# Kernel optimization log

Measured on AMD Instinct MI355X. Metric: run time of the kernel, lower is better.

## Reference

```python
import jax, jax.numpy as jnp
import numpy as np
import math

S = 64.0
M = 0.5
COS_M = math.cos(M)
SIN_M = math.sin(M)
TH = math.cos(math.pi - M)
MM = math.sin(math.pi - M) * M
BATCH = 512
EMBED = 512
NUM_CLASSES = 100000

def setup_inputs() -> dict:
    key = jax.random.key(0)
    k1, k2, k3 = jax.random.split(key, 3)
    inp = jax.random.normal(k1, (BATCH, EMBED), dtype=jnp.float32)
    label = jax.random.randint(k2, (BATCH,), 0, NUM_CLASSES, dtype=jnp.int64)
    # xavier_uniform_ on [num_classes, embedding_size]
    limit = math.sqrt(6.0 / (NUM_CLASSES + EMBED))
    weight = jax.random.uniform(k3, (NUM_CLASSES, EMBED), dtype=jnp.float32,
                                minval=-limit, maxval=limit)
    return {"input": inp, "label": label, "weight": weight}


def reference(input, label, weight):
    # F.normalize(weight) along dim=1 (eps=1e-12), then F.linear
    w_norm = weight / jnp.maximum(jnp.linalg.norm(weight, axis=1, keepdims=True), 1e-12)
    cosine = input @ w_norm.T  # [B, C]
    sine = jnp.sqrt(jnp.clip(1.0 - cosine * cosine, 0.0, 1.0))
    phi = cosine * COS_M - sine * SIN_M
    phi = jnp.where(cosine > TH, phi, cosine - MM)
    one_hot = jax.nn.one_hot(label, NUM_CLASSES, dtype=cosine.dtype)  # [B, C]
    output = (one_hot * phi + (1.0 - one_hot) * cosine) * S
    logp = jax.nn.log_softmax(output, axis=-1)
    # NLLLoss with mean reduction
    loss = -jnp.mean(jnp.take_along_axis(logp, label[:, None], axis=1)[:, 0])
    return (output, loss)
```

## Files before the change

### kernel.cpp

```cpp
#include <hip/hip_runtime.h>

#define NCLS   100000
#define CPAD   100096
#define EMB    512
#define BATCH  512
#define NBN    782
#define NJ     1564

#define S_F     64.0f
#define COS_M_F 0.8775825619f
#define SIN_M_F 0.4794255386f
#define TH_F   (-0.8775825619f)
#define MM_F    0.2397127693f

#define WS_ABF   0ull
#define WS_PMAX  524288ull
#define WS_PSUM  3727360ull
#define WS_NLL   6930432ull
#define WS_EXACT 6932480ull
#define WS_INV   6934528ull
#define WS_WBF   7334912ull

typedef unsigned short ushort_t;
typedef __attribute__((ext_vector_type(8))) short bf16x8;
typedef __attribute__((ext_vector_type(4))) float floatx4;

__device__ __forceinline__ unsigned short f2bf(float f) {
    union { float f; unsigned int u; } c; c.f = f;
    unsigned int r = c.u + 0x7FFFu + ((c.u >> 16) & 1u);
    return (unsigned short)(r >> 16);
}

__device__ __forceinline__ void load_lds16(const void* g, void* l) {
    __builtin_amdgcn_global_load_lds(
        (const __attribute__((address_space(1))) void*)g,
        (__attribute__((address_space(3))) void*)l, 16, 0, 0);
}

__device__ __forceinline__ int xcd_swizzle(int b0, int nwg) {
    const int q = nwg >> 3, r = nwg & 7;
    const int x = b0 & 7, o = b0 >> 3;
    const int base = (x < r) ? x * (q + 1) : r * (q + 1) + (x - r) * q;
    return base + o;
}

__global__ __launch_bounds__(256) void cvt_input_kernel(
    const float* __restrict__ in, ushort_t* __restrict__ Abf) {
    int gid = blockIdx.x * 256 + threadIdx.x;
    float4 f = ((const float4*)in)[gid];
    uint2 u;
    u.x = (unsigned)f2bf(f.x) | ((unsigned)f2bf(f.y) << 16);
    u.y = (unsigned)f2bf(f.z) | ((unsigned)f2bf(f.w) << 16);
    ((uint2*)Abf)[gid] = u;
}

__global__ __launch_bounds__(256) void exact_label_kernel(
    const float* __restrict__ input, const float* __restrict__ W,
    const int* __restrict__ label, float* __restrict__ exact_val) {
    const int t = threadIdx.x;
    const int lane = t & 63;
    const int row = blockIdx.x * 4 + (t >> 6);
    const int lab = label[row];
    const float4* ip = (const float4*)(input + (size_t)row * EMB);
    const float4* wp = (const float4*)(W + (size_t)lab * EMB);
    float4 a0 = ip[lane], a1 = ip[64 + lane];
    float4 b0 = wp[lane], b1 = wp[64 + lane];
    float dot = a0.x*b0.x + a0.y*b0.y + a0.z*b0.z + a0.w*b0.w
              + a1.x*b1.x + a1.y*b1.y + a1.z*b1.z + a1.w*b1.w;
    float ssq = b0.x*b0.x + b0.y*b0.y + b0.z*b0.z + b0.w*b0.w
              + b1.x*b1.x + b1.y*b1.y + b1.z*b1.z + b1.w*b1.w;
    #pragma unroll
    for (int msk = 1; msk < 64; msk <<= 1) {
        dot += __shfl_xor(dot, msk);
        ssq += __shfl_xor(ssq, msk);
    }
    if (lane == 0) {
        float c = dot / fmaxf(sqrtf(ssq), 1e-12f);
        float sine = sqrtf(fmaxf(1.0f - c * c, 0.0f));
        float phi = c * COS_M_F - sine * SIN_M_F;
        phi = (c > TH_F) ? phi : (c - MM_F);
        exact_val[row] = S_F * phi;
    }
}

__global__ __launch_bounds__(256) void norms_chunk_kernel(
    const float* __restrict__ W, ushort_t* __restrict__ Wbfc, int cls0) {
    const int t = threadIdx.x, lane = t & 63;
    const int rl = blockIdx.x * 4 + (t >> 6);
    const int r = cls0 + rl;
    float4 f0 = make_float4(0.f, 0.f, 0.f, 0.f);
    float4 f1 = make_float4(0.f, 0.f, 0.f, 0.f);
    float ssq = 0.f;
    if (r < NCLS) {
        const float4* rp = (const float4*)(W + (size_t)r * EMB);
        f0 = rp[lane * 2];
        f1 = rp[lane * 2 + 1];
        ssq = f0.x*f0.x + f0.y*f0.y + f0.z*f0.z + f0.w*f0.w
            + f1.x*f1.x + f1.y*f1.y + f1.z*f1.z + f1.w*f1.w;
    }
    #pragma unroll
    for (int msk = 1; msk < 64; msk <<= 1) ssq += __shfl_xor(ssq, msk);
    float inv = 0.f;
    if (r < NCLS) inv = 1.0f / fmaxf(sqrtf(ssq), 1e-12f);
    uint4 u;
    u.x = (unsigned)f2bf(f0.x*inv) | ((unsigned)f2bf(f0.y*inv) << 16);
    u.y = (unsigned)f2bf(f0.z*inv) | ((unsigned)f2bf(f0.w*inv) << 16);
    u.z = (unsigned)f2bf(f1.x*inv) | ((unsigned)f2bf(f1.y*inv) << 16);
    u.w = (unsigned)f2bf(f1.z*inv) | ((unsigned)f2bf(f1.w*inv) << 16);
    ((uint4*)(Wbfc + (size_t)rl * EMB))[lane] = u;
}

__global__ __launch_bounds__(256) void norms_inv_kernel(
    const float* __restrict__ W, float* __restrict__ inv_norm) {
    const int t = threadIdx.x, lane = t & 63;
    const int r = blockIdx.x * 4 + (t >> 6);
    float ssq = 0.f;
    if (r < NCLS) {
        const float4* rp = (const float4*)(W + (size_t)r * EMB);
        float4 f0 = rp[lane * 2], f1 = rp[lane * 2 + 1];
        ssq = f0.x*f0.x + f0.y*f0.y + f0.z*f0.z + f0.w*f0.w
            + f1.x*f1.x + f1.y*f1.y + f1.z*f1.z + f1.w*f1.w;
    }
    #pragma unroll
    for (int msk = 1; msk < 64; msk <<= 1) ssq += __shfl_xor(ssq, msk);
    if (lane == 0 && r < CPAD)
        inv_norm[r] = (r < NCLS) ? 1.0f / fmaxf(sqrtf(ssq), 1e-12f) : 0.f;
}

template <int BSRC>
__global__ __launch_bounds__(256) void gemm_kernel(
    const ushort_t* __restrict__ Abf,
    const float*    __restrict__ Wfp,
    const ushort_t* __restrict__ Wbfc,
    const float*    __restrict__ inv_norm,
    const int*      __restrict__ label,
    const float*    __restrict__ exact_val,
    float*          __restrict__ out,
    float* __restrict__ pmax, float* __restrict__ psum,
    int nblk0) {
    __shared__ ushort_t As[128 * 64];
    __shared__ ushort_t Bs[128 * 64];

    const int t = threadIdx.x;
    const int lane = t & 63, wid = t >> 6;
    const int wr = wid >> 1, wc = wid & 1;
    const int wg = xcd_swizzle(blockIdx.x, gridDim.x);
    const int mblk = wg & 3, nblkL = wg >> 2;
    const int m0 = mblk * 128;
    const int nblk = nblk0 + nblkL;
    const int c0 = nblk * 128;

    floatx4 acc[4][4] = {};

    for (int k0 = 0; k0 < EMB; k0 += 64) {
        __syncthreads();
        #pragma unroll
        for (int r = 0; r < 4; ++r) {
            const int i = r * 256 + t;
            const int row = i >> 3;
            const int ls = (i & 7) ^ (row & 7);
            const ushort_t* gp = Abf + (size_t)(m0 + row) * EMB + k0 + (ls << 3);
            load_lds16(gp, (char*)As + (size_t)(r * 256 + wid * 64) * 16);
        }
        if constexpr (BSRC == 0) {
            #pragma unroll
            for (int r = 0; r < 4; ++r) {
                const int i = r * 256 + t;
                const int row = i >> 3;
                const int ls = (i & 7) ^ (row & 7);
                const ushort_t* gp = Wbfc + (size_t)(nblkL * 128 + row) * EMB + k0 + (ls << 3);
                load_lds16(gp, (char*)Bs + (size_t)(r * 256 + wid * 64) * 16);
            }
        } else {
            #pragma unroll
            for (int r = 0; r < 4; ++r) {
                const int i = r * 256 + t;
                const int row = i >> 3;
                const int ls = i & 7;
                const int c = c0 + row;
                bf16x8 v = {0, 0, 0, 0, 0, 0, 0, 0};
                if (c < NCLS) {
                    const float* gp = Wfp + (size_t)c * EMB + k0 + (ls << 3);
                    float4 a = ((const float4*)gp)[0];
                    float4 b = ((const float4*)gp)[1];
                    v[0] = (short)f2bf(a.x); v[1] = (short)f2bf(a.y);
                    v[2] = (short)f2bf(a.z); v[3] = (short)f2bf(a.w);
                    v[4] = (short)f2bf(b.x); v[5] = (short)f2bf(b.y);
                    v[6] = (short)f2bf(b.z); v[7] = (short)f2bf(b.w);
                }
                *(bf16x8*)((char*)Bs + (size_t)row * 128 + ((ls ^ (row & 7)) << 4)) = v;
            }
        }
        __syncthreads();
        const int fr = lane & 15, q = lane >> 4, sx = fr & 7;
        #pragma unroll
        for (int kk = 0; kk < 2; ++kk) {
            const int lslot = kk * 4 + q;
            bf16x8 af[4], bw[4];
            #pragma unroll
            for (int m = 0; m < 4; ++m) {
                const int row = wr * 64 + m * 16 + fr;
                af[m] = *(const bf16x8*)((const char*)As + (size_t)row * 128 + ((lslot ^ sx) << 4));
            }
            #pragma unroll
            for (int n = 0; n < 4; ++n) {
                const int row = wc * 64 + n * 16 + fr;
                bw[n] = *(const bf16x8*)((const char*)Bs + (size_t)row * 128 + ((lslot ^ sx) << 4));
            }
            #pragma unroll
            for (int m = 0; m < 4; ++m)
                #pragma unroll
                for (int n = 0; n < 4; ++n)
                    acc[m][n] = __builtin_amdgcn_mfma_f32_16x16x32_bf16(
                        af[m], bw[n], acc[m][n], 0, 0, 0);
        }
    }

    const int fr = lane & 15, q = lane >> 4;
    const int jcol = (nblk << 1) | wc;
    #pragma unroll
    for (int m = 0; m < 4; ++m) {
        #pragma unroll
        for (int j = 0; j < 4; ++j) {
            const int grow = m0 + wr * 64 + m * 16 + q * 4 + j;
            const int lab = label[grow];
            const float exv = exact_val[grow];
            float o[4]; int cc[4];
            float vmax = -1e30f;
            #pragma unroll
            for (int n = 0; n < 4; ++n) {
                const int col = c0 + wc * 64 + n * 16 + fr;
                float cosv = acc[m][n][j];
                if (BSRC == 1) cosv *= inv_norm[col];
                float val = (col == lab) ? exv : (S_F * cosv);
                o[n] = val; cc[n] = col;
                if (col < NCLS) {
                    __builtin_nontemporal_store(val, &out[(size_t)grow * NCLS + col]);
                    vmax = fmaxf(vmax, val);
                }
            }
            #pragma unroll
            for (int msk = 1; msk < 16; msk <<= 1)
                vmax = fmaxf(vmax, __shfl_xor(vmax, msk));
            float vsum = 0.0f;
            #pragma unroll
            for (int n = 0; n < 4; ++n)
                if (cc[n] < NCLS) vsum += __expf(o[n] - vmax);
            #pragma unroll
            for (int msk = 1; msk < 16; msk <<= 1)
                vsum += __shfl_xor(vsum, msk);
            if (fr == 0) {
                pmax[(size_t)grow * NJ + jcol] = vmax;
                psum[(size_t)grow * NJ + jcol] = vsum;
            }
        }
    }
}

__global__ __launch_bounds__(256) void row_lse_kernel(
    const float* __restrict__ pmax, const float* __restrict__ psum,
    const float* __restrict__ out, const int* __restrict__ label,
    float* __restrict__ nll) {
    const int row = blockIdx.x;
    const int t = threadIdx.x;
    float m = -1e30f, s = 0.f;
    for (int j = t; j < NJ; j += 256) {
        float pm = pmax[(size_t)row * NJ + j];
        float ps = psum[(size_t)row * NJ + j];
        float nm = fmaxf(m, pm);
        s = s * __expf(m - nm) + ps * __expf(pm - nm);
        m = nm;
    }
    #pragma unroll
    for (int msk = 1; msk < 64; msk <<= 1) {
        float om = __shfl_xor(m, msk), os = __shfl_xor(s, msk);
        float nm = fmaxf(m, om);
        s = s * __expf(m - nm) + os * __expf(om - nm);
        m = nm;
    }
    __shared__ float sm[4], ss[4];
    const int lane = t & 63, wid = t >> 6;
    if (lane == 0) { sm[wid] = m; ss[wid] = s; }
    __syncthreads();
    if (t == 0) {
        float M = sm[0], SS = ss[0];
        #pragma unroll
        for (int w = 1; w < 4; ++w) {
            float nm = fmaxf(M, sm[w]);
            SS = SS * __expf(M - nm) + ss[w] * __expf(sm[w] - nm);
            M = nm;
        }
        float lse = M + logf(SS);
        float tgt = out[(size_t)row * NCLS + label[row]];
        nll[row] = lse - tgt;
    }
}

__global__ __launch_bounds__(512) void loss_kernel(
    const float* __restrict__ nll, float* __restrict__ out_loss) {
    const int t = threadIdx.x;
    float v = nll[t];
    #pragma unroll
    for (int msk = 1; msk < 64; msk <<= 1) v += __shfl_xor(v, msk);
    __shared__ float sv[8];
    if ((t & 63) == 0) sv[t >> 6] = v;
    __syncthreads();
    if (t == 0) {
        float s = 0.f;
        #pragma unroll
        for (int w = 0; w < 8; ++w) s += sv[w];
        out_loss[0] = s / 512.0f;
    }
}

extern "C" void kernel_launch(void* const* d_in, const int* in_sizes, int n_in,
                              void* d_out, int out_size, void* d_ws, size_t ws_size,
                              hipStream_t stream) {
    const float* input  = (const float*)d_in[0];
    const int*   label  = (const int*)d_in[1];
    const float* weight = (const float*)d_in[2];
    float* out = (float*)d_out;
    char* ws = (char*)d_ws;
    ushort_t* Abf  = (ushort_t*)(ws + WS_ABF);
    float*    pmax = (float*)(ws + WS_PMAX);
    float*    psum = (float*)(ws + WS_PSUM);
    float*    nll  = (float*)(ws + WS_NLL);
    float*    exv  = (float*)(ws + WS_EXACT);
    float*    invn = (float*)(ws + WS_INV);
    ushort_t* Wbf  = (ushort_t*)(ws + WS_WBF);

    size_t avail = ws_size > WS_WBF ? ws_size - WS_WBF : 0;
    int nch = 0, per = 0;
    const int cand[5] = {1, 2, 4, 8, 16};
    for (int ci = 0; ci < 5; ++ci) {
        int p = (NBN + cand[ci] - 1) / cand[ci];
        if ((size_t)p * 128 * EMB * 2 <= avail) { nch = cand[ci]; per = p; break; }
    }

    cvt_input_kernel<<<dim3(256), dim3(256), 0, stream>>>(input, Abf);
    exact_label_kernel<<<dim3(128), dim3(256), 0, stream>>>(input, weight, label, exv);

    if (nch) {
        for (int c = 0; c < nch; ++c) {
            const int nb0 = c * per;
            int pc = NBN - nb0; if (pc > per) pc = per;
            if (pc <= 0) break;
            norms_chunk_kernel<<<dim3(pc * 32), dim3(256), 0, stream>>>(
                weight, Wbf, nb0 * 128);
            gemm_kernel<0><<<dim3(4 * pc), dim3(256), 0, stream>>>(
                Abf, weight, Wbf, invn, label, exv, out, pmax, psum, nb0);
        }
    } else {
        norms_inv_kernel<<<dim3(CPAD / 4), dim3(256), 0, stream>>>(weight, invn);
        gemm_kernel<1><<<dim3(4 * NBN), dim3(256), 0, stream>>>(
            Abf, weight, Wbf, invn, label, exv, out, pmax, psum, 0);
    }
    row_lse_kernel<<<dim3(512), dim3(256), 0, stream>>>(pmax, psum, out, label, nll);
    loss_kernel<<<dim3(1), dim3(512), 0, stream>>>(nll, out + (out_size - 1));
}
```

Before: 510.6 us.

## Double-buffer GEMM LDS tiles, transpose partial-stat layout, drop nontemporal stores

The GEMM main loop now stages the next K-tile into a second LDS buffer while MFMAs run on the current one, with scheduling barriers, setprio hints and a launch bound of two blocks per CU. Output stores become regular instead of nontemporal. The per-tile max/sum partials are stored column-major (jcol*BATCH+row), and the row reduction kernel reads them in that order. The host now always splits the weight conversion into at least two chunks. Together these try to hide global-load latency and change memory access patterns, at the cost of doubled LDS use and possibly lower occupancy.

```diff
diff --git a/kernel.cpp b/kernel.cpp
--- a/kernel.cpp
+++ b/kernel.cpp
@@ -128,7 +128,7 @@
 }
 
 template <int BSRC>
-__global__ __launch_bounds__(256) void gemm_kernel(
+__global__ __launch_bounds__(256, 2) void gemm_kernel(
     const ushort_t* __restrict__ Abf,
     const float*    __restrict__ Wfp,
     const ushort_t* __restrict__ Wbfc,
@@ -138,8 +138,8 @@
     float*          __restrict__ out,
     float* __restrict__ pmax, float* __restrict__ psum,
     int nblk0) {
-    __shared__ ushort_t As[128 * 64];
-    __shared__ ushort_t Bs[128 * 64];
+    __shared__ ushort_t As[2][128 * 64];
+    __shared__ ushort_t Bs[2][128 * 64];
 
     const int t = threadIdx.x;
     const int lane = t & 63, wid = t >> 6;
@@ -152,68 +152,87 @@
 
     floatx4 acc[4][4] = {};
 
-    for (int k0 = 0; k0 < EMB; k0 += 64) {
-        __syncthreads();
+    auto stageA = [&](int buf, int k0) {
         #pragma unroll
         for (int r = 0; r < 4; ++r) {
             const int i = r * 256 + t;
             const int row = i >> 3;
             const int ls = (i & 7) ^ (row & 7);
-            const ushort_t* gp = Abf + (size_t)(m0 + row) * EMB + k0 + (ls << 3);
-            load_lds16(gp, (char*)As + (size_t)(r * 256 + wid * 64) * 16);
-        }
-        if constexpr (BSRC == 0) {
-            #pragma unroll
-            for (int r = 0; r < 4; ++r) {
-                const int i = r * 256 + t;
-                const int row = i >> 3;
-                const int ls = (i & 7) ^ (row & 7);
-                const ushort_t* gp = Wbfc + (size_t)(nblkL * 128 + row) * EMB + k0 + (ls << 3);
-                load_lds16(gp, (char*)Bs + (size_t)(r * 256 + wid * 64) * 16);
-            }
-        } else {
-            #pragma unroll
-            for (int r = 0; r < 4; ++r) {
-                const int i = r * 256 + t;
-                const int row = i >> 3;
-                const int ls = i & 7;
-                const int c = c0 + row;
-                bf16x8 v = {0, 0, 0, 0, 0, 0, 0, 0};
-                if (c < NCLS) {
-                    const float* gp = Wfp + (size_t)c * EMB + k0 + (ls << 3);
-                    float4 a = ((const float4*)gp)[0];
-                    float4 b = ((const float4*)gp)[1];
-                    v[0] = (short)f2bf(a.x); v[1] = (short)f2bf(a.y);
-                    v[2] = (short)f2bf(a.z); v[3] = (short)f2bf(a.w);
-                    v[4] = (short)f2bf(b.x); v[5] = (short)f2bf(b.y);
-                    v[6] = (short)f2bf(b.z); v[7] = (short)f2bf(b.w);
-                }
-                *(bf16x8*)((char*)Bs + (size_t)row * 128 + ((ls ^ (row & 7)) << 4)) = v;
-            }
-        }
-        __syncthreads();
-        const int fr = lane & 15, q = lane >> 4, sx = fr & 7;
+            load_lds16(Abf + (size_t)(m0 + row) * EMB + k0 + (ls << 3),
+                       (char*)As[buf] + (size_t)(r * 256 + wid * 64) * 16);
+        }
+    };
+    auto stageB0 = [&](int buf, int k0) {
+        #pragma unroll
+        for (int r = 0; r < 4; ++r) {
+            const int i = r * 256 + t;
+            const int row = i >> 3;
+            const int ls = (i & 7) ^ (row & 7);
+            load_lds16(Wbfc + (size_t)(nblkL * 128 + row) * EMB + k0 + (ls << 3),
+                       (char*)Bs[buf] + (size_t)(r * 256 + wid * 64) * 16);
+        }
+    };
+    auto stageB1 = [&](int buf, int k0) {
+        #pragma unroll
+        for (int r = 0; r < 4; ++r) {
+            const int i = r * 256 + t;
+            const int row = i >> 3;
+            const int ls = i & 7;
+            const int c = c0 + row;
+            bf16x8 v = {0, 0, 0, 0, 0, 0, 0, 0};
+            if (c < NCLS) {
+                const float* gp = Wfp + (size_t)c * EMB + k0 + (ls << 3);
+                float4 a = ((const float4*)gp)[0];
+                float4 b = ((const float4*)gp)[1];
+                v[0] = (short)f2bf(a.x); v[1] = (short)f2bf(a.y);
+                v[2] = (short)f2bf(a.z); v[3] = (short)f2bf(a.w);
+                v[4] = (short)f2bf(b.x); v[5] = (short)f2bf(b.y);
+                v[6] = (short)f2bf(b.z); v[7] = (short)f2bf(b.w);
+            }
+            *(bf16x8*)((char*)Bs[buf] + (size_t)row * 128 + ((ls ^ (row & 7)) << 4)) = v;
+        }
+    };
+
+    stageA(0, 0);
+    if constexpr (BSRC == 0) stageB0(0, 0); else stageB1(0, 0);
+    __syncthreads();
+
+    const int fr0 = lane & 15, q0 = lane >> 4, sx = fr0 & 7;
+
+    for (int kt = 0; kt < 8; ++kt) {
+        const int cur = kt & 1;
+        if (kt < 7) {
+            stageA(cur ^ 1, (kt + 1) * 64);
+            if constexpr (BSRC == 0) stageB0(cur ^ 1, (kt + 1) * 64);
+            else                     stageB1(cur ^ 1, (kt + 1) * 64);
+        }
+        __builtin_amdgcn_sched_barrier(0);
+        const char* Ab = (const char*)As[cur];
+        const char* Bb = (const char*)Bs[cur];
         #pragma unroll
         for (int kk = 0; kk < 2; ++kk) {
-            const int lslot = kk * 4 + q;
+            const int lslot = kk * 4 + q0;
             bf16x8 af[4], bw[4];
             #pragma unroll
             for (int m = 0; m < 4; ++m) {
-                const int row = wr * 64 + m * 16 + fr;
-                af[m] = *(const bf16x8*)((const char*)As + (size_t)row * 128 + ((lslot ^ sx) << 4));
+                const int row = wr * 64 + m * 16 + fr0;
+                af[m] = *(const bf16x8*)(Ab + (size_t)row * 128 + ((lslot ^ sx) << 4));
             }
             #pragma unroll
             for (int n = 0; n < 4; ++n) {
-                const int row = wc * 64 + n * 16 + fr;
-                bw[n] = *(const bf16x8*)((const char*)Bs + (size_t)row * 128 + ((lslot ^ sx) << 4));
-            }
+                const int row = wc * 64 + n * 16 + fr0;
+                bw[n] = *(const bf16x8*)(Bb + (size_t)row * 128 + ((lslot ^ sx) << 4));
+            }
+            __builtin_amdgcn_s_setprio(1);
             #pragma unroll
             for (int m = 0; m < 4; ++m)
                 #pragma unroll
                 for (int n = 0; n < 4; ++n)
                     acc[m][n] = __builtin_amdgcn_mfma_f32_16x16x32_bf16(
                         af[m], bw[n], acc[m][n], 0, 0, 0);
-        }
+            __builtin_amdgcn_s_setprio(0);
+        }
+        __syncthreads();
     }
 
     const int fr = lane & 15, q = lane >> 4;
@@ -235,7 +254,7 @@
                 float val = (col == lab) ? exv : (S_F * cosv);
                 o[n] = val; cc[n] = col;
                 if (col < NCLS) {
-                    __builtin_nontemporal_store(val, &out[(size_t)grow * NCLS + col]);
+                    out[(size_t)grow * NCLS + col] = val;
                     vmax = fmaxf(vmax, val);
                 }
             }
@@ -250,8 +269,8 @@
             for (int msk = 1; msk < 16; msk <<= 1)
                 vsum += __shfl_xor(vsum, msk);
             if (fr == 0) {
-                pmax[(size_t)grow * NJ + jcol] = vmax;
-                psum[(size_t)grow * NJ + jcol] = vsum;
+                pmax[(size_t)jcol * BATCH + grow] = vmax;
+                psum[(size_t)jcol * BATCH + grow] = vsum;
             }
         }
     }
@@ -265,8 +284,8 @@
     const int t = threadIdx.x;
     float m = -1e30f, s = 0.f;
     for (int j = t; j < NJ; j += 256) {
-        float pm = pmax[(size_t)row * NJ + j];
-        float ps = psum[(size_t)row * NJ + j];
+        float pm = pmax[(size_t)j * BATCH + row];
+        float ps = psum[(size_t)j * BATCH + row];
         float nm = fmaxf(m, pm);
         s = s * __expf(m - nm) + ps * __expf(pm - nm);
         m = nm;
@@ -331,8 +350,8 @@
 
     size_t avail = ws_size > WS_WBF ? ws_size - WS_WBF : 0;
     int nch = 0, per = 0;
-    const int cand[5] = {1, 2, 4, 8, 16};
-    for (int ci = 0; ci < 5; ++ci) {
+    const int cand[4] = {2, 4, 8, 16};
+    for (int ci = 0; ci < 4; ++ci) {
         int p = (NBN + cand[ci] - 1) / cand[ci];
         if ((size_t)p * 128 * EMB * 2 <= avail) { nch = cand[ci]; per = p; break; }
     }
```

Result: faster. 485.1 us (-5.0%).
